# Performance work log

Measured on AMD Instinct MI355X. Metric: run time of the kernel, lower is better.

## Reference

```python
import jax, jax.numpy as jnp
import numpy as np

N = 20000       # nodes
E = 640000      # random edges (self-loops appended -> E + N total)
G = 64          # graphs in batch
F_IN = 114
H1 = 3          # heads in layer 1
D2 = 128        # output_dim of layer 2
NEG = 0.2       # GATConv leaky_relu negative slope


def setup_inputs() -> dict:
    key = jax.random.key(0)
    ks = jax.random.split(key, 20)
    x = jax.random.normal(ks[0], (N, F_IN), jnp.float32)
    src = jax.random.randint(ks[1], (E,), 0, N, jnp.int32)
    dst = jax.random.randint(ks[2], (E,), 0, N, jnp.int32)
    loop = jnp.arange(N, dtype=jnp.int32)  # PyG add_self_loops=True
    edge_index = jnp.stack([jnp.concatenate([src, loop]),
                            jnp.concatenate([dst, loop])])
    batch = (jnp.arange(N) * G // N).astype(jnp.int32)  # every graph non-empty

    def lin(k, i, o):
        return jax.random.normal(k, (i, o), jnp.float32) * (1.0 / np.sqrt(i))

    return {
        "x": x, "edge_index": edge_index, "batch": batch,
        # GATConv 1: 114 -> 114 per head, 3 heads, concat
        "W1": lin(ks[3], F_IN, H1 * F_IN),
        "a_src1": jax.random.normal(ks[4], (H1, F_IN), jnp.float32) * 0.1,
        "a_dst1": jax.random.normal(ks[5], (H1, F_IN), jnp.float32) * 0.1,
        "b1": jnp.zeros((H1 * F_IN,), jnp.float32),
        # GATConv 2: 342 -> 128, 1 head
        "W2": lin(ks[6], H1 * F_IN, D2),
        "a_src2": jax.random.normal(ks[7], (1, D2), jnp.float32) * 0.1,
        "a_dst2": jax.random.normal(ks[8], (1, D2), jnp.float32) * 0.1,
        "b2": jnp.zeros((D2,), jnp.float32),
        # MLP head
        "Wg": lin(ks[9], D2, 64),  "bg": jnp.zeros((64,), jnp.float32),
        "Wf1": lin(ks[10], 64, 32), "bf1": jnp.zeros((32,), jnp.float32),
        "Wf2": lin(ks[11], 32, 16), "bf2": jnp.zeros((16,), jnp.float32),
        "Wo": lin(ks[12], 16, 1),   "bo": jnp.zeros((1,), jnp.float32),
    }


def gat_conv(x, edge_index, W, a_src, a_dst, b, heads, dim):
    """PyG GATConv (self-loops already in edge_index, eval mode)."""
    n = x.shape[0]
    h = (x @ W).reshape(n, heads, dim)             # [N,H,D]
    src, dst = edge_index[0], edge_index[1]
    alpha_s = jnp.sum(h * a_src, axis=-1)          # [N,H]
    alpha_d = jnp.sum(h * a_dst, axis=-1)          # [N,H]
    e = jax.nn.leaky_relu(alpha_s[src] + alpha_d[dst], NEG)  # [E,H]
    # segment softmax over destination nodes
    m = jax.ops.segment_max(e, dst, num_segments=n)
    ex = jnp.exp(e - m[dst])
    s = jax.ops.segment_sum(ex, dst, num_segments=n)
    alpha = ex / s[dst]                            # [E,H]
    out = jax.ops.segment_sum(h[src] * alpha[..., None], dst, num_segments=n)
    return out.reshape(n, heads * dim) + b


def reference(x, edge_index, batch, W1, a_src1, a_dst1, b1,
              W2, a_src2, a_dst2, b2, Wg, bg, Wf1, bf1, Wf2, bf2, Wo, bo):
    h = jax.nn.elu(gat_conv(x, edge_index, W1, a_src1, a_dst1, b1, H1, F_IN))
    h = jax.nn.relu(gat_conv(h, edge_index, W2, a_src2, a_dst2, b2, 1, D2))
    g = jax.ops.segment_max(h, batch, num_segments=G)   # global max pool [G,128]
    g = jax.nn.relu(g @ Wg + bg)
    g = jax.nn.relu(g @ Wf1 + bf1)
    g = jax.nn.relu(g @ Wf2 + bf2)
    return g @ Wo + bo                                  # [G,1]
```

## Files before the change

### kernel.cpp

```cpp
#include <hip/hip_runtime.h>

#define NN 20000
#define EE 660000
#define GG 64
#define FIN 114
#define H1 3
#define F1 342
#define D2 128
#define NEG 0.2f

typedef __attribute__((ext_vector_type(8))) short short8v;
typedef __attribute__((ext_vector_type(4))) float f32x4;
typedef unsigned short ushort_t;

__device__ inline unsigned fenc(float f) {
    unsigned u = __float_as_uint(f);
    return (u & 0x80000000u) ? ~u : (u | 0x80000000u);
}
__device__ inline float fdec(unsigned u) {
    return (u & 0x80000000u) ? __uint_as_float(u & 0x7FFFFFFFu) : __uint_as_float(~u);
}
__device__ inline float lrelu(float x) { return x > 0.f ? x : NEG * x; }

__device__ inline void split2(float x, ushort_t& hi, ushort_t& lo) {
    unsigned u = __float_as_uint(x);
    unsigned uh = u & 0xFFFF0000u;
    hi = (ushort_t)(uh >> 16);
    float r = x - __uint_as_float(uh);
    unsigned v = __float_as_uint(r);
    unsigned vh = (v + 0x7FFFu + ((v >> 16) & 1u)) & 0xFFFF0000u;
    lo = (ushort_t)(vh >> 16);
}

__global__ void k_wa(const float* __restrict__ W1, const float* __restrict__ aS,
                     const float* __restrict__ aD, float* __restrict__ was,
                     float* __restrict__ wad) {
    int tid = blockIdx.x * 256 + threadIdx.x;
    if (tid >= 2 * FIN * H1) return;
    int which = tid >= FIN * H1;
    int i = which ? tid - FIN * H1 : tid;
    int k = i / H1, h = i % H1;
    const float* a = which ? aD : aS;
    float s = 0.f;
    for (int d = 0; d < FIN; d++) s += W1[k * F1 + h * FIN + d] * a[h * FIN + d];
    (which ? wad : was)[i] = s;
}

__global__ void k_prep1m(const float* __restrict__ W1, ushort_t* __restrict__ W1Th,
                         ushort_t* __restrict__ W1Tl) {
    int tid = blockIdx.x * 256 + threadIdx.x;
    if (tid >= H1 * 128 * 128) return;
    int h = tid / (128 * 128);
    int rem = tid & (128 * 128 - 1);
    int c = rem >> 7, k = rem & 127;
    float v = (c < FIN && k < FIN) ? W1[k * F1 + h * FIN + c] : 0.f;
    ushort_t hi, lo;
    split2(v, hi, lo);
    W1Th[tid] = hi;
    W1Tl[tid] = lo;
}

__global__ void k_prep2m(const float* __restrict__ W2, ushort_t* __restrict__ W2Th,
                         ushort_t* __restrict__ W2Tl) {
    int tid = blockIdx.x * 256 + threadIdx.x;
    if (tid >= 128 * 384) return;
    int c = tid / 384;
    int hk = tid - c * 384;
    int h = hk >> 7, k = hk & 127;
    float v = (k < FIN) ? W2[(h * FIN + k) * D2 + c] : 0.f;
    ushort_t hi, lo;
    split2(v, hi, lo);
    W2Th[tid] = hi;
    W2Tl[tid] = lo;
}

__global__ __launch_bounds__(256) void k_alpha1x(const float* __restrict__ x,
                                                 const float* __restrict__ was,
                                                 const float* __restrict__ wad,
                                                 float* __restrict__ as1,
                                                 float* __restrict__ ad1) {
    int n = blockIdx.x * 4 + (threadIdx.x >> 6);
    int l = threadIdx.x & 63;
    if (n >= NN) return;
    float x0 = x[n * FIN + l];
    float x1 = (l < FIN - 64) ? x[n * FIN + 64 + l] : 0.f;
    float s[H1], d[H1];
#pragma unroll
    for (int h = 0; h < H1; h++) {
        float w0s = was[l * H1 + h], w0d = wad[l * H1 + h];
        float w1s = (l < FIN - 64) ? was[(64 + l) * H1 + h] : 0.f;
        float w1d = (l < FIN - 64) ? wad[(64 + l) * H1 + h] : 0.f;
        s[h] = x0 * w0s + x1 * w1s;
        d[h] = x0 * w0d + x1 * w1d;
    }
#pragma unroll
    for (int o = 32; o > 0; o >>= 1) {
#pragma unroll
        for (int h = 0; h < H1; h++) {
            s[h] += __shfl_down(s[h], o);
            d[h] += __shfl_down(d[h], o);
        }
    }
    if (l == 0) {
#pragma unroll
        for (int h = 0; h < H1; h++) {
            as1[n * H1 + h] = s[h];
            ad1[n * H1 + h] = d[h];
        }
    }
}

__global__ void k_count(const int* __restrict__ dst, int* __restrict__ cnt) {
    int e = blockIdx.x * 256 + threadIdx.x;
    if (e < EE) atomicAdd(&cnt[dst[e]], 1);
}

__global__ __launch_bounds__(1024) void k_scan(const int* __restrict__ cnt,
                                               int* __restrict__ off) {
    __shared__ int part[1024];
    int t = threadIdx.x;
    const int CH = 20;
    int loc[CH];
    int s = 0;
    int base = t * CH;
    for (int i = 0; i < CH; i++) {
        int idx = base + i;
        int v = (idx < NN) ? cnt[idx] : 0;
        loc[i] = s;
        s += v;
    }
    part[t] = s;
    __syncthreads();
    for (int d = 1; d < 1024; d <<= 1) {
        int v = (t >= d) ? part[t - d] : 0;
        __syncthreads();
        part[t] += v;
        __syncthreads();
    }
    int pre = (t == 0) ? 0 : part[t - 1];
    for (int i = 0; i < CH; i++) {
        int idx = base + i;
        if (idx < NN) off[idx] = pre + loc[i];
    }
    if (t == 1023) off[NN] = part[1023];
}

__global__ void k_scatter(const int* __restrict__ src, const int* __restrict__ dst,
                          const int* __restrict__ off, int* __restrict__ cur,
                          int* __restrict__ csr_src) {
    int e = blockIdx.x * 256 + threadIdx.x;
    if (e < EE) {
        int d = dst[e];
        int pos = off[d] + atomicAdd(&cur[d], 1);
        csr_src[pos] = src[e];
    }
}

__global__ __launch_bounds__(128) void k_aggx(const float* __restrict__ x,
                                              const float* __restrict__ as1,
                                              const float* __restrict__ ad1,
                                              const int* __restrict__ off,
                                              const int* __restrict__ csr_src,
                                              ushort_t* __restrict__ xgh,
                                              ushort_t* __restrict__ xgl) {
    int n = blockIdx.x, t = threadIdx.x;
    int e0 = off[n], e1 = off[n + 1];
    float adv0 = ad1[n * H1 + 0], adv1 = ad1[n * H1 + 1], adv2 = ad1[n * H1 + 2];
    __shared__ int ssrc[64];
    __shared__ float sw[64][H1];
    __shared__ float red[64][H1];
    float acc0 = 0.f, acc1 = 0.f, acc2 = 0.f;
    float ps0 = 0.f, ps1 = 0.f, ps2 = 0.f;
    for (int base = e0; base < e1; base += 64) {
        int c = min(64, e1 - base);
        __syncthreads();
        if (t < c) {
            int s = csr_src[base + t];
            ssrc[t] = s;
            float w0 = __expf(lrelu(as1[s * H1 + 0] + adv0));
            float w1 = __expf(lrelu(as1[s * H1 + 1] + adv1));
            float w2 = __expf(lrelu(as1[s * H1 + 2] + adv2));
            sw[t][0] = w0; sw[t][1] = w1; sw[t][2] = w2;
            ps0 += w0; ps1 += w1; ps2 += w2;
        }
        __syncthreads();
        if (t < FIN) {
            int j = 0;
            for (; j + 4 <= c; j += 4) {
                int s0 = ssrc[j + 0], s1 = ssrc[j + 1];
                int s2 = ssrc[j + 2], s3 = ssrc[j + 3];
                float v0 = x[(size_t)s0 * FIN + t];
                float v1 = x[(size_t)s1 * FIN + t];
                float v2 = x[(size_t)s2 * FIN + t];
                float v3 = x[(size_t)s3 * FIN + t];
                acc0 += v0 * sw[j + 0][0]; acc1 += v0 * sw[j + 0][1]; acc2 += v0 * sw[j + 0][2];
                acc0 += v1 * sw[j + 1][0]; acc1 += v1 * sw[j + 1][1]; acc2 += v1 * sw[j + 1][2];
                acc0 += v2 * sw[j + 2][0]; acc1 += v2 * sw[j + 2][1]; acc2 += v2 * sw[j + 2][2];
                acc0 += v3 * sw[j + 3][0]; acc1 += v3 * sw[j + 3][1]; acc2 += v3 * sw[j + 3][2];
            }
            for (; j < c; j++) {
                float xv = x[(size_t)ssrc[j] * FIN + t];
                acc0 += xv * sw[j][0];
                acc1 += xv * sw[j][1];
                acc2 += xv * sw[j][2];
            }
        }
    }
    __syncthreads();
    if (t < 64) { red[t][0] = ps0; red[t][1] = ps1; red[t][2] = ps2; }
    __syncthreads();
    for (int sr = 32; sr > 0; sr >>= 1) {
        if (t < sr) {
            red[t][0] += red[t + sr][0];
            red[t][1] += red[t + sr][1];
            red[t][2] += red[t + sr][2];
        }
        __syncthreads();
    }
    float i0 = 1.f / red[0][0], i1 = 1.f / red[0][1], i2 = 1.f / red[0][2];
    float v0 = (t < FIN) ? acc0 * i0 : 0.f;
    float v1 = (t < FIN) ? acc1 * i1 : 0.f;
    float v2 = (t < FIN) ? acc2 * i2 : 0.f;
    ushort_t hi, lo;
    split2(v0, hi, lo);
    xgh[(size_t)0 * NN * 128 + n * 128 + t] = hi;
    xgl[(size_t)0 * NN * 128 + n * 128 + t] = lo;
    split2(v1, hi, lo);
    xgh[(size_t)1 * NN * 128 + n * 128 + t] = hi;
    xgl[(size_t)1 * NN * 128 + n * 128 + t] = lo;
    split2(v2, hi, lo);
    xgh[(size_t)2 * NN * 128 + n * 128 + t] = hi;
    xgl[(size_t)2 * NN * 128 + n * 128 + t] = lo;
}

__global__ __launch_bounds__(128) void k_agg2f(const float* __restrict__ h2,
                                               const float* __restrict__ as2,
                                               const float* __restrict__ ad2,
                                               const int* __restrict__ off,
                                               const int* __restrict__ csr_src,
                                               const float* __restrict__ b2,
                                               unsigned* __restrict__ poolbuf) {
    int n = blockIdx.x, t = threadIdx.x;
    int e0 = off[n], e1 = off[n + 1];
    float adv = ad2[n];
    __shared__ int ssrc[64];
    __shared__ float sw[64];
    __shared__ float red[64];
    float acc = 0.f, ps = 0.f;
    for (int base = e0; base < e1; base += 64) {
        int c = min(64, e1 - base);
        __syncthreads();
        if (t < c) {
            int s = csr_src[base + t];
            ssrc[t] = s;
            float w = __expf(lrelu(as2[s] + adv));
            sw[t] = w;
            ps += w;
        }
        __syncthreads();
        int j = 0;
        for (; j + 8 <= c; j += 8) {
            float v0 = h2[(size_t)ssrc[j + 0] * D2 + t];
            float v1 = h2[(size_t)ssrc[j + 1] * D2 + t];
            float v2 = h2[(size_t)ssrc[j + 2] * D2 + t];
            float v3 = h2[(size_t)ssrc[j + 3] * D2 + t];
            float v4 = h2[(size_t)ssrc[j + 4] * D2 + t];
            float v5 = h2[(size_t)ssrc[j + 5] * D2 + t];
            float v6 = h2[(size_t)ssrc[j + 6] * D2 + t];
            float v7 = h2[(size_t)ssrc[j + 7] * D2 + t];
            acc += v0 * sw[j + 0]; acc += v1 * sw[j + 1];
            acc += v2 * sw[j + 2]; acc += v3 * sw[j + 3];
            acc += v4 * sw[j + 4]; acc += v5 * sw[j + 5];
            acc += v6 * sw[j + 6]; acc += v7 * sw[j + 7];
        }
        for (; j < c; j++) acc += h2[(size_t)ssrc[j] * D2 + t] * sw[j];
    }
    __syncthreads();
    if (t < 64) red[t] = ps;
    __syncthreads();
    for (int sr = 32; sr > 0; sr >>= 1) {
        if (t < sr) red[t] += red[t + sr];
        __syncthreads();
    }
    float v = fmaxf(acc / red[0] + b2[t], 0.f);
    int g = (int)(((long long)n * GG) / NN);
    atomicMax(&poolbuf[g * D2 + t], fenc(v));
}

__global__ __launch_bounds__(256) void k_gemm1m(const ushort_t* __restrict__ xgh,
                                                const ushort_t* __restrict__ xgl,
                                                const ushort_t* __restrict__ W1Th,
                                                const ushort_t* __restrict__ W1Tl,
                                                const float* __restrict__ b1,
                                                ushort_t* __restrict__ h1hi,
                                                ushort_t* __restrict__ h1lo) {
    int h = blockIdx.y;
    int rb = blockIdx.x * 128;
    int tid = threadIdx.x;
    int w = tid >> 6, l = tid & 63;
    int m = l & 15, g = l >> 4;
    int r0 = rb + w * 32 + m;
    int r1 = r0 + 16;
    bool ok0 = (r0 < NN), ok1 = (r1 < NN);
    const ushort_t* xh = xgh + (size_t)h * NN * 128;
    const ushort_t* xl = xgl + (size_t)h * NN * 128;
    const ushort_t* Bhg = W1Th + (size_t)h * 128 * 128;
    const ushort_t* Blg = W1Tl + (size_t)h * 128 * 128;
    const short8v z8 = {0, 0, 0, 0, 0, 0, 0, 0};
    __shared__ __align__(16) ushort_t BsH[128 * 40];
    __shared__ __align__(16) ushort_t BsL[128 * 40];
    f32x4 acc0[8], acc1[8];
#pragma unroll
    for (int j = 0; j < 8; j++) {
        acc0[j] = (f32x4){0.f, 0.f, 0.f, 0.f};
        acc1[j] = (f32x4){0.f, 0.f, 0.f, 0.f};
    }
    for (int k0i = 0; k0i < 4; k0i++) {
        int k0 = k0i * 32;
        __syncthreads();
        int ka = k0 + g * 8;
        short8v a0h = ok0 ? *(const short8v*)(xh + (size_t)r0 * 128 + ka) : z8;
        short8v a0l = ok0 ? *(const short8v*)(xl + (size_t)r0 * 128 + ka) : z8;
        short8v a1h = ok1 ? *(const short8v*)(xh + (size_t)r1 * 128 + ka) : z8;
        short8v a1l = ok1 ? *(const short8v*)(xl + (size_t)r1 * 128 + ka) : z8;
#pragma unroll
        for (int it = 0; it < 2; it++) {
            int idx = tid + it * 256;
            int c = idx >> 2, q = idx & 3;
            size_t go = (size_t)c * 128 + k0 + q * 8;
            int lo_off = c * 40 + q * 8;
            *(short8v*)(&BsH[lo_off]) = *(const short8v*)(Bhg + go);
            *(short8v*)(&BsL[lo_off]) = *(const short8v*)(Blg + go);
        }
        __syncthreads();
#pragma unroll
        for (int j = 0; j < 8; j++) {
            int c = j * 16 + m;
            short8v bh = *(const short8v*)(&BsH[c * 40 + g * 8]);
            short8v bl = *(const short8v*)(&BsL[c * 40 + g * 8]);
            acc0[j] = __builtin_amdgcn_mfma_f32_16x16x32_bf16(a0h, bh, acc0[j], 0, 0, 0);
            acc1[j] = __builtin_amdgcn_mfma_f32_16x16x32_bf16(a1h, bh, acc1[j], 0, 0, 0);
            acc0[j] = __builtin_amdgcn_mfma_f32_16x16x32_bf16(a0h, bl, acc0[j], 0, 0, 0);
            acc1[j] = __builtin_amdgcn_mfma_f32_16x16x32_bf16(a1h, bl, acc1[j], 0, 0, 0);
            acc0[j] = __builtin_amdgcn_mfma_f32_16x16x32_bf16(a0l, bh, acc0[j], 0, 0, 0);
            acc1[j] = __builtin_amdgcn_mfma_f32_16x16x32_bf16(a1l, bh, acc1[j], 0, 0, 0);
        }
    }
    ushort_t* Hh = h1hi + (size_t)h * NN * 128;
    ushort_t* Hl = h1lo + (size_t)h * NN * 128;
#pragma unroll
    for (int j = 0; j < 8; j++) {
        int c = j * 16 + m;
        float bv = (c < FIN) ? b1[h * FIN + c] : 0.f;
#pragma unroll
        for (int r = 0; r < 4; r++) {
            int orow0 = rb + w * 32 + g * 4 + r;
            int orow1 = orow0 + 16;
            if (orow0 < NN) {
                float v = acc0[j][r] + bv;
                v = v > 0.f ? v : expm1f(v);
                ushort_t hi = 0, lo = 0;
                if (c < FIN) split2(v, hi, lo);
                Hh[(size_t)orow0 * 128 + c] = hi;
                Hl[(size_t)orow0 * 128 + c] = lo;
            }
            if (orow1 < NN) {
                float v = acc1[j][r] + bv;
                v = v > 0.f ? v : expm1f(v);
                ushort_t hi = 0, lo = 0;
                if (c < FIN) split2(v, hi, lo);
                Hh[(size_t)orow1 * 128 + c] = hi;
                Hl[(size_t)orow1 * 128 + c] = lo;
            }
        }
    }
}

__global__ __launch_bounds__(256) void k_gemm2m(const ushort_t* __restrict__ h1hi,
                                                const ushort_t* __restrict__ h1lo,
                                                const ushort_t* __restrict__ W2Th,
                                                const ushort_t* __restrict__ W2Tl,
                                                float* __restrict__ h2) {
    int rb = blockIdx.x * 128;
    int tid = threadIdx.x;
    int w = tid >> 6, l = tid & 63;
    int m = l & 15, g = l >> 4;
    int r0 = rb + w * 32 + m;
    int r1 = r0 + 16;
    bool ok0 = (r0 < NN), ok1 = (r1 < NN);
    const short8v z8 = {0, 0, 0, 0, 0, 0, 0, 0};
    __shared__ __align__(16) ushort_t BsH[128 * 40];
    __shared__ __align__(16) ushort_t BsL[128 * 40];
    f32x4 acc0[8], acc1[8];
#pragma unroll
    for (int j = 0; j < 8; j++) {
        acc0[j] = (f32x4){0.f, 0.f, 0.f, 0.f};
        acc1[j] = (f32x4){0.f, 0.f, 0.f, 0.f};
    }
    for (int k0i = 0; k0i < 12; k0i++) {
        int k0 = k0i * 32;
        __syncthreads();
        int hh = k0 >> 7;
        int kc = (k0 & 127) + g * 8;
        size_t a0o = ((size_t)hh * NN + (size_t)(ok0 ? r0 : 0)) * 128 + kc;
        size_t a1o = ((size_t)hh * NN + (size_t)(ok1 ? r1 : 0)) * 128 + kc;
        short8v a0h = ok0 ? *(const short8v*)(h1hi + a0o) : z8;
        short8v a0l = ok0 ? *(const short8v*)(h1lo + a0o) : z8;
        short8v a1h = ok1 ? *(const short8v*)(h1hi + a1o) : z8;
        short8v a1l = ok1 ? *(const short8v*)(h1lo + a1o) : z8;
#pragma unroll
        for (int it = 0; it < 2; it++) {
            int idx = tid + it * 256;
            int c = idx >> 2, q = idx & 3;
            size_t go = (size_t)c * 384 + k0 + q * 8;
            int lo_off = c * 40 + q * 8;
            *(short8v*)(&BsH[lo_off]) = *(const short8v*)(W2Th + go);
            *(short8v*)(&BsL[lo_off]) = *(const short8v*)(W2Tl + go);
        }
        __syncthreads();
#pragma unroll
        for (int j = 0; j < 8; j++) {
            int c = j * 16 + m;
            short8v bh = *(const short8v*)(&BsH[c * 40 + g * 8]);
            short8v bl = *(const short8v*)(&BsL[c * 40 + g * 8]);
            acc0[j] = __builtin_amdgcn_mfma_f32_16x16x32_bf16(a0h, bh, acc0[j], 0, 0, 0);
            acc1[j] = __builtin_amdgcn_mfma_f32_16x16x32_bf16(a1h, bh, acc1[j], 0, 0, 0);
            acc0[j] = __builtin_amdgcn_mfma_f32_16x16x32_bf16(a0h, bl, acc0[j], 0, 0, 0);
            acc1[j] = __builtin_amdgcn_mfma_f32_16x16x32_bf16(a1h, bl, acc1[j], 0, 0, 0);
            acc0[j] = __builtin_amdgcn_mfma_f32_16x16x32_bf16(a0l, bh, acc0[j], 0, 0, 0);
            acc1[j] = __builtin_amdgcn_mfma_f32_16x16x32_bf16(a1l, bh, acc1[j], 0, 0, 0);
        }
    }
#pragma unroll
    for (int j = 0; j < 8; j++) {
        int c = j * 16 + m;
#pragma unroll
        for (int r = 0; r < 4; r++) {
            int orow0 = rb + w * 32 + g * 4 + r;
            int orow1 = orow0 + 16;
            if (orow0 < NN) h2[(size_t)orow0 * D2 + c] = acc0[j][r];
            if (orow1 < NN) h2[(size_t)orow1 * D2 + c] = acc1[j][r];
        }
    }
}

__global__ __launch_bounds__(256) void k_alpha2(const float* __restrict__ h2,
                                                const float* __restrict__ aS,
                                                const float* __restrict__ aD,
                                                float* __restrict__ as2,
                                                float* __restrict__ ad2) {
    int n = blockIdx.x * 4 + (threadIdx.x >> 6);
    int l = threadIdx.x & 63;
    if (n >= NN) return;
    float v0 = h2[(size_t)n * D2 + l], v1 = h2[(size_t)n * D2 + 64 + l];
    float ps = v0 * aS[l] + v1 * aS[64 + l];
    float pd = v0 * aD[l] + v1 * aD[64 + l];
    for (int o = 32; o > 0; o >>= 1) {
        ps += __shfl_down(ps, o);
        pd += __shfl_down(pd, o);
    }
    if (l == 0) {
        as2[n] = ps;
        ad2[n] = pd;
    }
}

__global__ __launch_bounds__(128) void k_mlp(const unsigned* __restrict__ poolbuf,
                                             const float* __restrict__ Wg,
                                             const float* __restrict__ bg,
                                             const float* __restrict__ Wf1,
                                             const float* __restrict__ bf1,
                                             const float* __restrict__ Wf2,
                                             const float* __restrict__ bf2,
                                             const float* __restrict__ Wo,
                                             const float* __restrict__ bo,
                                             float* __restrict__ out) {
    int g = blockIdx.x;
    int t = threadIdx.x;
    __shared__ float pool[D2];
    __shared__ float a1[64];
    __shared__ float a2[32];
    __shared__ float a3[16];
    pool[t] = fdec(poolbuf[g * D2 + t]);
    __syncthreads();
    if (t < 64) {
        float acc = bg[t];
        for (int k = 0; k < D2; k++) acc += pool[k] * Wg[k * 64 + t];
        a1[t] = fmaxf(acc, 0.f);
    }
    __syncthreads();
    if (t < 32) {
        float acc = bf1[t];
        for (int k = 0; k < 64; k++) acc += a1[k] * Wf1[k * 32 + t];
        a2[t] = fmaxf(acc, 0.f);
    }
    __syncthreads();
    if (t < 16) {
        float acc = bf2[t];
        for (int k = 0; k < 32; k++) acc += a2[k] * Wf2[k * 16 + t];
        a3[t] = fmaxf(acc, 0.f);
    }
    __syncthreads();
    if (t == 0) {
        float acc = bo[0];
        for (int k = 0; k < 16; k++) acc += a3[k] * Wo[k];
        out[g] = acc;
    }
}

extern "C" void kernel_launch(void* const* d_in, const int* in_sizes, int n_in,
                              void* d_out, int out_size, void* d_ws, size_t ws_size,
                              hipStream_t stream) {
    const float* x = (const float*)d_in[0];
    const int* ei = (const int*)d_in[1];
    const float* W1 = (const float*)d_in[3];
    const float* aS1 = (const float*)d_in[4];
    const float* aD1 = (const float*)d_in[5];
    const float* b1 = (const float*)d_in[6];
    const float* W2 = (const float*)d_in[7];
    const float* aS2 = (const float*)d_in[8];
    const float* aD2 = (const float*)d_in[9];
    const float* b2 = (const float*)d_in[10];
    const float* Wg = (const float*)d_in[11];
    const float* bg = (const float*)d_in[12];
    const float* Wf1 = (const float*)d_in[13];
    const float* bf1 = (const float*)d_in[14];
    const float* Wf2 = (const float*)d_in[15];
    const float* bf2 = (const float*)d_in[16];
    const float* Wo = (const float*)d_in[17];
    const float* bo = (const float*)d_in[18];
    float* out = (float*)d_out;

    const int* src = ei;
    const int* dst = ei + EE;

    char* ws = (char*)d_ws;
    size_t o = 0;
    auto alloc = [&](size_t bytes) -> char* {
        char* p = ws + o;
        o += (bytes + 255) & ~(size_t)255;
        return p;
    };
    float* was = (float*)alloc((size_t)FIN * H1 * 4);
    float* wad = (float*)alloc((size_t)FIN * H1 * 4);
    ushort_t* W1Th = (ushort_t*)alloc((size_t)H1 * 128 * 128 * 2);
    ushort_t* W1Tl = (ushort_t*)alloc((size_t)H1 * 128 * 128 * 2);
    ushort_t* W2Th = (ushort_t*)alloc((size_t)128 * 384 * 2);
    ushort_t* W2Tl = (ushort_t*)alloc((size_t)128 * 384 * 2);
    float* as1 = (float*)alloc((size_t)NN * H1 * 4);
    float* ad1 = (float*)alloc((size_t)NN * H1 * 4);
    int* cnt = (int*)alloc((size_t)NN * 4);
    int* off = (int*)alloc((size_t)(NN + 1) * 4);
    int* cur = (int*)alloc((size_t)NN * 4);
    int* csr_src = (int*)alloc((size_t)EE * 4);
    ushort_t* xgh = (ushort_t*)alloc((size_t)H1 * NN * 128 * 2);
    ushort_t* xgl = (ushort_t*)alloc((size_t)H1 * NN * 128 * 2);
    ushort_t* h1hi = (ushort_t*)alloc((size_t)H1 * NN * 128 * 2);
    ushort_t* h1lo = (ushort_t*)alloc((size_t)H1 * NN * 128 * 2);
    float* h2 = (float*)alloc((size_t)NN * D2 * 4);
    float* as2 = (float*)alloc((size_t)NN * 4);
    float* ad2 = (float*)alloc((size_t)NN * 4);
    unsigned* poolbuf = (unsigned*)alloc((size_t)GG * D2 * 4);
    (void)ws_size;

    hipMemsetAsync(cnt, 0, (size_t)NN * 4, stream);
    hipMemsetAsync(cur, 0, (size_t)NN * 4, stream);
    hipMemsetAsync(poolbuf, 0, (size_t)GG * D2 * 4, stream);

    const int EB = (EE + 255) / 256;

    k_wa<<<(2 * FIN * H1 + 255) / 256, 256, 0, stream>>>(W1, aS1, aD1, was, wad);
    k_prep1m<<<(H1 * 128 * 128 + 255) / 256, 256, 0, stream>>>(W1, W1Th, W1Tl);
    k_prep2m<<<(128 * 384 + 255) / 256, 256, 0, stream>>>(W2, W2Th, W2Tl);
    k_alpha1x<<<(NN + 3) / 4, 256, 0, stream>>>(x, was, wad, as1, ad1);
    k_count<<<EB, 256, 0, stream>>>(dst, cnt);
    k_scan<<<1, 1024, 0, stream>>>(cnt, off);
    k_scatter<<<EB, 256, 0, stream>>>(src, dst, off, cur, csr_src);
    k_aggx<<<NN, 128, 0, stream>>>(x, as1, ad1, off, csr_src, xgh, xgl);
    k_gemm1m<<<dim3((NN + 127) / 128, H1), 256, 0, stream>>>(xgh, xgl, W1Th, W1Tl, b1, h1hi, h1lo);
    k_gemm2m<<<(NN + 127) / 128, 256, 0, stream>>>(h1hi, h1lo, W2Th, W2Tl, h2);
    k_alpha2<<<(NN + 3) / 4, 256, 0, stream>>>(h2, aS2, aD2, as2, ad2);
    k_agg2f<<<NN, 128, 0, stream>>>(h2, as2, ad2, off, csr_src, b2, poolbuf);
    k_mlp<<<GG, 128, 0, stream>>>(poolbuf, Wg, bg, Wf1, bf1, Wf2, bf2, Wo, bo, out);
}
```

Baseline: 278.0 us.

## Fuse layer-2 attention logits into GEMM epilogue and split edges across waves

The separate alpha2 kernel is removed. The source and destination attention dot products are computed in the gemm2 epilogue from the MFMA accumulators, reduced with lane shuffles across the 16 column lanes, which saves one launch and one re-read of h2. The layer-2 aggregation kernel is also restructured: its two waves each take alternate edges and load float2 per lane covering all 128 columns. A shared-memory sum combines the two waves, and the weight-sum tree reduction becomes a wave shuffle. This halves the gather instructions per edge but adds a cross-wave reduction, and only 64 threads do the final atomics.

Result: slower. 289.6 us (+4.2%).

```diff
diff --git a/kernel.cpp b/kernel.cpp
--- a/kernel.cpp
+++ b/kernel.cpp
@@ -241,50 +241,62 @@
                                                const float* __restrict__ b2,
                                                unsigned* __restrict__ poolbuf) {
     int n = blockIdx.x, t = threadIdx.x;
+    int w = t >> 6, l = t & 63;
+    int col0 = l * 2;
     int e0 = off[n], e1 = off[n + 1];
     float adv = ad2[n];
     __shared__ int ssrc[64];
     __shared__ float sw[64];
-    __shared__ float red[64];
-    float acc = 0.f, ps = 0.f;
+    __shared__ float red[2][64][2];
+    __shared__ float ssum;
+    float acc0 = 0.f, acc1 = 0.f;
+    float ps = 0.f;
     for (int base = e0; base < e1; base += 64) {
         int c = min(64, e1 - base);
         __syncthreads();
         if (t < c) {
             int s = csr_src[base + t];
             ssrc[t] = s;
-            float w = __expf(lrelu(as2[s] + adv));
-            sw[t] = w;
-            ps += w;
-        }
-        __syncthreads();
-        int j = 0;
+            float wv = __expf(lrelu(as2[s] + adv));
+            sw[t] = wv;
+            ps += wv;
+        }
+        __syncthreads();
+        int j = w;
         for (; j + 8 <= c; j += 8) {
-            float v0 = h2[(size_t)ssrc[j + 0] * D2 + t];
-            float v1 = h2[(size_t)ssrc[j + 1] * D2 + t];
-            float v2 = h2[(size_t)ssrc[j + 2] * D2 + t];
-            float v3 = h2[(size_t)ssrc[j + 3] * D2 + t];
-            float v4 = h2[(size_t)ssrc[j + 4] * D2 + t];
-            float v5 = h2[(size_t)ssrc[j + 5] * D2 + t];
-            float v6 = h2[(size_t)ssrc[j + 6] * D2 + t];
-            float v7 = h2[(size_t)ssrc[j + 7] * D2 + t];
-            acc += v0 * sw[j + 0]; acc += v1 * sw[j + 1];
-            acc += v2 * sw[j + 2]; acc += v3 * sw[j + 3];
-            acc += v4 * sw[j + 4]; acc += v5 * sw[j + 5];
-            acc += v6 * sw[j + 6]; acc += v7 * sw[j + 7];
-        }
-        for (; j < c; j++) acc += h2[(size_t)ssrc[j] * D2 + t] * sw[j];
-    }
-    __syncthreads();
-    if (t < 64) red[t] = ps;
-    __syncthreads();
-    for (int sr = 32; sr > 0; sr >>= 1) {
-        if (t < sr) red[t] += red[t + sr];
-        __syncthreads();
-    }
-    float v = fmaxf(acc / red[0] + b2[t], 0.f);
-    int g = (int)(((long long)n * GG) / NN);
-    atomicMax(&poolbuf[g * D2 + t], fenc(v));
+            const float2 v0 = *(const float2*)(h2 + (size_t)ssrc[j] * D2 + col0);
+            const float2 v1 = *(const float2*)(h2 + (size_t)ssrc[j + 2] * D2 + col0);
+            const float2 v2 = *(const float2*)(h2 + (size_t)ssrc[j + 4] * D2 + col0);
+            const float2 v3 = *(const float2*)(h2 + (size_t)ssrc[j + 6] * D2 + col0);
+            acc0 += v0.x * sw[j];     acc1 += v0.y * sw[j];
+            acc0 += v1.x * sw[j + 2]; acc1 += v1.y * sw[j + 2];
+            acc0 += v2.x * sw[j + 4]; acc1 += v2.y * sw[j + 4];
+            acc0 += v3.x * sw[j + 6]; acc1 += v3.y * sw[j + 6];
+        }
+        for (; j < c; j += 2) {
+            const float2 v = *(const float2*)(h2 + (size_t)ssrc[j] * D2 + col0);
+            acc0 += v.x * sw[j];
+            acc1 += v.y * sw[j];
+        }
+    }
+    if (t < 64) {
+#pragma unroll
+        for (int o = 32; o > 0; o >>= 1) ps += __shfl_down(ps, o);
+        if (t == 0) ssum = ps;
+    }
+    red[w][l][0] = acc0;
+    red[w][l][1] = acc1;
+    __syncthreads();
+    if (t < 64) {
+        float r0 = red[0][l][0] + red[1][l][0];
+        float r1 = red[0][l][1] + red[1][l][1];
+        float inv = 1.f / ssum;
+        int gidx = (int)(((long long)n * GG) / NN);
+        float v0 = fmaxf(r0 * inv + b2[col0], 0.f);
+        float v1 = fmaxf(r1 * inv + b2[col0 + 1], 0.f);
+        atomicMax(&poolbuf[gidx * D2 + col0], fenc(v0));
+        atomicMax(&poolbuf[gidx * D2 + col0 + 1], fenc(v1));
+    }
 }
 
 __global__ __launch_bounds__(256) void k_gemm1m(const ushort_t* __restrict__ xgh,
@@ -380,7 +392,11 @@
                                                 const ushort_t* __restrict__ h1lo,
                                                 const ushort_t* __restrict__ W2Th,
                                                 const ushort_t* __restrict__ W2Tl,
-                                                float* __restrict__ h2) {
+                                                const float* __restrict__ aS2,
+                                                const float* __restrict__ aD2,
+                                                float* __restrict__ h2,
+                                                float* __restrict__ as2,
+                                                float* __restrict__ ad2) {
     int rb = blockIdx.x * 128;
     int tid = threadIdx.x;
     int w = tid >> 6, l = tid & 63;
@@ -442,26 +458,35 @@
             if (orow1 < NN) h2[(size_t)orow1 * D2 + c] = acc1[j][r];
         }
     }
-}
-
-__global__ __launch_bounds__(256) void k_alpha2(const float* __restrict__ h2,
-                                                const float* __restrict__ aS,
-                                                const float* __restrict__ aD,
-                                                float* __restrict__ as2,
-                                                float* __restrict__ ad2) {
-    int n = blockIdx.x * 4 + (threadIdx.x >> 6);
-    int l = threadIdx.x & 63;
-    if (n >= NN) return;
-    float v0 = h2[(size_t)n * D2 + l], v1 = h2[(size_t)n * D2 + 64 + l];
-    float ps = v0 * aS[l] + v1 * aS[64 + l];
-    float pd = v0 * aD[l] + v1 * aD[64 + l];
-    for (int o = 32; o > 0; o >>= 1) {
-        ps += __shfl_down(ps, o);
-        pd += __shfl_down(pd, o);
-    }
-    if (l == 0) {
-        as2[n] = ps;
-        ad2[n] = pd;
+    float sv[8], dv[8];
+#pragma unroll
+    for (int j = 0; j < 8; j++) {
+        sv[j] = aS2[j * 16 + m];
+        dv[j] = aD2[j * 16 + m];
+    }
+#pragma unroll
+    for (int r = 0; r < 4; r++) {
+        float s0 = 0.f, d0 = 0.f, s1 = 0.f, d1 = 0.f;
+#pragma unroll
+        for (int j = 0; j < 8; j++) {
+            s0 += acc0[j][r] * sv[j];
+            d0 += acc0[j][r] * dv[j];
+            s1 += acc1[j][r] * sv[j];
+            d1 += acc1[j][r] * dv[j];
+        }
+#pragma unroll
+        for (int o = 1; o < 16; o <<= 1) {
+            s0 += __shfl_xor(s0, o);
+            d0 += __shfl_xor(d0, o);
+            s1 += __shfl_xor(s1, o);
+            d1 += __shfl_xor(d1, o);
+        }
+        int orow0 = rb + w * 32 + g * 4 + r;
+        int orow1 = orow0 + 16;
+        if (m == 0) {
+            if (orow0 < NN) { as2[orow0] = s0; ad2[orow0] = d0; }
+            if (orow1 < NN) { as2[orow1] = s1; ad2[orow1] = d1; }
+        }
     }
 }
 
@@ -578,8 +603,7 @@
     k_scatter<<<EB, 256, 0, stream>>>(src, dst, off, cur, csr_src);
     k_aggx<<<NN, 128, 0, stream>>>(x, as1, ad1, off, csr_src, xgh, xgl);
     k_gemm1m<<<dim3((NN + 127) / 128, H1), 256, 0, stream>>>(xgh, xgl, W1Th, W1Tl, b1, h1hi, h1lo);
-    k_gemm2m<<<(NN + 127) / 128, 256, 0, stream>>>(h1hi, h1lo, W2Th, W2Tl, h2);
-    k_alpha2<<<(NN + 3) / 4, 256, 0, stream>>>(h2, aS2, aD2, as2, ad2);
+    k_gemm2m<<<(NN + 127) / 128, 256, 0, stream>>>(h1hi, h1lo, W2Th, W2Tl, aS2, aD2, h2, as2, ad2);
     k_agg2f<<<NN, 128, 0, stream>>>(h2, as2, ad2, off, csr_src, b2, poolbuf);
     k_mlp<<<GG, 128, 0, stream>>>(poolbuf, Wg, bg, Wf1, bf1, Wf2, bf2, Wo, bo, out);
 }
```
